# Optimization experiments

Hardware: AMD Instinct MI355X
Metric: run time of the kernel (lower is better)

Reference implementation:

```python
import jax, jax.numpy as jnp
import numpy as np

TOKENS = 8192
MODEL_DIM = 4096
PROMPT_DIM = 64
NUM_EXPERTS = 8
TOP_K = 2
EPS = float(np.finfo(np.float32).eps)


def setup_inputs() -> dict:
    key = jax.random.key(0)
    k1, k2, k3 = jax.random.split(key, 3)
    x = jax.random.normal(k1, (TOKENS, MODEL_DIM), dtype=jnp.float32)
    prompt = jax.random.normal(k2, (TOKENS, PROMPT_DIM), dtype=jnp.float32)
    # gate linear: Linear(model_dim + prompt_dim, num_experts, bias=True)
    W = jax.random.normal(k3, (MODEL_DIM + PROMPT_DIM, NUM_EXPERTS), dtype=jnp.float32) * 0.02
    b = jnp.zeros((NUM_EXPERTS,), dtype=jnp.float32)
    return {"x": x, "prompt": prompt, "W": W, "b": b}


def reference(x, prompt, W, b):
    # eval path: no jitter, no noise (self.training is False)
    logits = jnp.concatenate([x, prompt], axis=-1) @ W + b          # [T, E]
    _, topk_idx = jax.lax.top_k(logits, TOP_K)                      # [T, K]
    masks = jax.nn.one_hot(topk_idx, NUM_EXPERTS, dtype=jnp.float32)  # [T, K, E]
    gates = jax.nn.softmax(logits, axis=-1)                         # [T, E]
    gates_s = jnp.einsum("te,tke->tk", gates, masks)               # masked gather-sum
    if TOP_K > 1:
        denom = jnp.maximum(gates_s.sum(axis=-1, keepdims=True), EPS)
        gates_s = gates_s / denom
    # masks[:, i] == masks_se[i], gates_s[:, i] == gates_s[i] in the torch code
    return masks, gates_s
```

## Files before the change

kernel.cpp:

```cpp
#include <hip/hip_runtime.h>
#include <math.h>

#define NE 8
#define KDIM 4096
#define PDIM 64
#define WROWS (KDIM + PDIM)
#define EPS_F32 1.1920929e-07f
#define NCHUNK 16
#define TPW 2
#define WAVES 16
#define ROWF4 (WROWS / 4)
#define LDSF4 (NE * ROWF4)

typedef float f4 __attribute__((ext_vector_type(4)));

__global__ __launch_bounds__(256)
void transpose_w(const float* __restrict__ W, float* __restrict__ Wt) {
    const int k = blockIdx.x * 256 + threadIdx.x;
    if (k < WROWS) {
        float v[NE];
#pragma unroll
        for (int e = 0; e < NE; ++e) v[e] = W[(size_t)k * NE + e];
#pragma unroll
        for (int e = 0; e < NE; ++e) Wt[(size_t)e * WROWS + k] = v[e];
    }
}

__global__ __launch_bounds__(1024, 4)
void topk_gate(const float* __restrict__ x,
               const float* __restrict__ prompt,
               const float* __restrict__ Wt,
               const float* __restrict__ b,
               float* __restrict__ out,
               int tokens)
{
    __shared__ f4 wlds[LDSF4];

    const int tid  = threadIdx.x;
    const int lane = tid & 63;
    const int wid  = tid >> 6;

    {
        const f4* wt4 = (const f4*)Wt;
        for (int i = tid; i < LDSF4; i += WAVES * 64)
            wlds[i] = wt4[i];
    }
    __syncthreads();

    const int tbase = (blockIdx.x * WAVES + wid) * TPW;
    const int phase = (blockIdx.x * 5) & 15;

    float acc[TPW][NE];
#pragma unroll
    for (int t = 0; t < TPW; ++t)
#pragma unroll
        for (int e = 0; e < NE; ++e) acc[t][e] = 0.f;

    const f4* xr0 = (const f4*)(x + (size_t)tbase * KDIM);
    const f4* xr1 = (const f4*)(x + (size_t)(tbase + 1) * KDIM);

    f4 xb[3][TPW];

    auto cidx = [&](int c) { return ((c + phase) & 15) * 64 + lane; };

    {
        const int k0 = cidx(0);
        xb[0][0] = __builtin_nontemporal_load(xr0 + k0);
        xb[0][1] = __builtin_nontemporal_load(xr1 + k0);
        const int k1 = cidx(1);
        xb[1][0] = __builtin_nontemporal_load(xr0 + k1);
        xb[1][1] = __builtin_nontemporal_load(xr1 + k1);
    }

#pragma unroll
    for (int c = 0; c < NCHUNK; ++c) {
        if (c + 2 < NCHUNK) {
            const int kx = cidx(c + 2);
            xb[(c + 2) % 3][0] = __builtin_nontemporal_load(xr0 + kx);
            xb[(c + 2) % 3][1] = __builtin_nontemporal_load(xr1 + kx);
        }

        const int kw = cidx(c);
        f4 wb[NE];
#pragma unroll
        for (int e = 0; e < NE; ++e)
            wb[e] = wlds[e * ROWF4 + kw];

        const int s = c % 3;
#pragma unroll
        for (int t = 0; t < TPW; ++t)
#pragma unroll
            for (int e = 0; e < NE; ++e) {
                const f4 xv = xb[s][t];
                acc[t][e] = fmaf(xv.x, wb[e].x, acc[t][e]);
                acc[t][e] = fmaf(xv.y, wb[e].y, acc[t][e]);
                acc[t][e] = fmaf(xv.z, wb[e].z, acc[t][e]);
                acc[t][e] = fmaf(xv.w, wb[e].w, acc[t][e]);
            }
    }

    if (lane < 16) {
        f4 pv[TPW];
#pragma unroll
        for (int t = 0; t < TPW; ++t)
            pv[t] = *((const f4*)(prompt + (size_t)(tbase + t) * PDIM) + lane);
#pragma unroll
        for (int e = 0; e < NE; ++e) {
            const f4 wv = wlds[e * ROWF4 + (KDIM / 4) + lane];
#pragma unroll
            for (int t = 0; t < TPW; ++t) {
                acc[t][e] = fmaf(pv[t].x, wv.x, acc[t][e]);
                acc[t][e] = fmaf(pv[t].y, wv.y, acc[t][e]);
                acc[t][e] = fmaf(pv[t].z, wv.z, acc[t][e]);
                acc[t][e] = fmaf(pv[t].w, wv.w, acc[t][e]);
            }
        }
    }

#pragma unroll
    for (int t = 0; t < TPW; ++t)
#pragma unroll
        for (int e = 0; e < NE; ++e) {
            float v = acc[t][e];
#pragma unroll
            for (int off = 32; off >= 1; off >>= 1)
                v += __shfl_xor(v, off, 64);
            acc[t][e] = v;
        }

    const int tt = (lane >> 4) & 1;
    const int kk = (lane >> 3) & 1;
    const int ee = lane & 7;

    float lg[NE];
#pragma unroll
    for (int e = 0; e < NE; ++e) {
        const float v = (tt == 0) ? acc[0][e] : acc[1][e];
        lg[e] = v + b[e];
    }

    float v0 = lg[0]; int i0 = 0;
#pragma unroll
    for (int e = 1; e < NE; ++e)
        if (lg[e] > v0) { v0 = lg[e]; i0 = e; }
    float v1 = (i0 == 0) ? lg[1] : lg[0];
    int   i1 = (i0 == 0) ? 1 : 0;
#pragma unroll
    for (int e = 0; e < NE; ++e)
        if (e != i0 && lg[e] > v1) { v1 = lg[e]; i1 = e; }

    float s = 0.f;
#pragma unroll
    for (int e = 0; e < NE; ++e) s += __expf(lg[e] - v0);
    const float g0 = 1.0f / s;
    const float g1 = __expf(v1 - v0) / s;
    const float denom = fmaxf(g0 + g1, EPS_F32);

    if (lane < 32) {
        const int sel = kk ? i1 : i0;
        const int t_global = tbase + tt;
        out[(size_t)t_global * 16 + kk * 8 + ee] = (ee == sel) ? 1.0f : 0.0f;

        if ((lane & 15) < 2) {
            const float g = (ee == 0) ? (g0 / denom) : (g1 / denom);
            out[(size_t)tokens * 16 + (size_t)t_global * 2 + ee] = g;
        }
    }
}

extern "C" void kernel_launch(void* const* d_in, const int* in_sizes, int n_in,
                              void* d_out, int out_size, void* d_ws, size_t ws_size,
                              hipStream_t stream) {
    const float* x      = (const float*)d_in[0];
    const float* prompt = (const float*)d_in[1];
    const float* W      = (const float*)d_in[2];
    const float* b      = (const float*)d_in[3];
    float* out          = (float*)d_out;
    float* Wt           = (float*)d_ws;

    const int tokens = in_sizes[0] / KDIM;

    hipLaunchKernelGGL(transpose_w, dim3((WROWS + 255) / 256), dim3(256), 0, stream,
                       W, Wt);
    hipLaunchKernelGGL(topk_gate, dim3(tokens / (WAVES * TPW)), dim3(WAVES * 64),
                       0, stream, x, prompt, Wt, b, out, tokens);
}
```

Before: 202.4 us.

## Fuse weight transpose into gate kernel and prefetch x before LDS fill

Removes the separate transpose kernel launch. Each block now reads the original row-major W and scatters it transposed into shared memory. The first two x chunks are issued before the LDS fill, so global loads overlap the weight staging. The main loop now walks 8 groups of two 64-lane chunks instead of 16 chunks, with more x registers in flight. The trade-offs are scalar LDS stores, which may cause bank conflicts, higher register pressure, and every block redoing the transpose work.

```diff
diff --git a/kernel.cpp b/kernel.cpp
--- a/kernel.cpp
+++ b/kernel.cpp
@@ -6,97 +6,121 @@
 #define PDIM 64
 #define WROWS (KDIM + PDIM)
 #define EPS_F32 1.1920929e-07f
-#define NCHUNK 16
+#define NG 8
 #define TPW 2
 #define WAVES 16
 #define ROWF4 (WROWS / 4)
-#define LDSF4 (NE * ROWF4)
+#define LDSF (NE * WROWS)
 
 typedef float f4 __attribute__((ext_vector_type(4)));
-
-__global__ __launch_bounds__(256)
-void transpose_w(const float* __restrict__ W, float* __restrict__ Wt) {
-    const int k = blockIdx.x * 256 + threadIdx.x;
-    if (k < WROWS) {
-        float v[NE];
-#pragma unroll
-        for (int e = 0; e < NE; ++e) v[e] = W[(size_t)k * NE + e];
-#pragma unroll
-        for (int e = 0; e < NE; ++e) Wt[(size_t)e * WROWS + k] = v[e];
-    }
-}
 
 __global__ __launch_bounds__(1024, 4)
 void topk_gate(const float* __restrict__ x,
                const float* __restrict__ prompt,
-               const float* __restrict__ Wt,
+               const float* __restrict__ W,
                const float* __restrict__ b,
                float* __restrict__ out,
                int tokens)
 {
-    __shared__ f4 wlds[LDSF4];
+    __shared__ float wlds[LDSF];
 
     const int tid  = threadIdx.x;
     const int lane = tid & 63;
     const int wid  = tid >> 6;
 
-    {
-        const f4* wt4 = (const f4*)Wt;
-        for (int i = tid; i < LDSF4; i += WAVES * 64)
-            wlds[i] = wt4[i];
-    }
-    __syncthreads();
-
     const int tbase = (blockIdx.x * WAVES + wid) * TPW;
-    const int phase = (blockIdx.x * 5) & 15;
-
-    float acc[TPW][NE];
-#pragma unroll
-    for (int t = 0; t < TPW; ++t)
-#pragma unroll
-        for (int e = 0; e < NE; ++e) acc[t][e] = 0.f;
+    const int phase = (blockIdx.x * 5) & 7;
 
     const f4* xr0 = (const f4*)(x + (size_t)tbase * KDIM);
     const f4* xr1 = (const f4*)(x + (size_t)(tbase + 1) * KDIM);
 
-    f4 xb[3][TPW];
-
-    auto cidx = [&](int c) { return ((c + phase) & 15) * 64 + lane; };
+    f4 xb[3][TPW][2];
+
+    auto gidx = [&](int g, int j) {
+        return ((g + phase) & 7) * 128 + j * 64 + lane;
+    };
 
     {
-        const int k0 = cidx(0);
-        xb[0][0] = __builtin_nontemporal_load(xr0 + k0);
-        xb[0][1] = __builtin_nontemporal_load(xr1 + k0);
-        const int k1 = cidx(1);
-        xb[1][0] = __builtin_nontemporal_load(xr0 + k1);
-        xb[1][1] = __builtin_nontemporal_load(xr1 + k1);
-    }
-
-#pragma unroll
-    for (int c = 0; c < NCHUNK; ++c) {
-        if (c + 2 < NCHUNK) {
-            const int kx = cidx(c + 2);
-            xb[(c + 2) % 3][0] = __builtin_nontemporal_load(xr0 + kx);
-            xb[(c + 2) % 3][1] = __builtin_nontemporal_load(xr1 + kx);
-        }
-
-        const int kw = cidx(c);
-        f4 wb[NE];
-#pragma unroll
-        for (int e = 0; e < NE; ++e)
-            wb[e] = wlds[e * ROWF4 + kw];
-
-        const int s = c % 3;
-#pragma unroll
-        for (int t = 0; t < TPW; ++t)
-#pragma unroll
-            for (int e = 0; e < NE; ++e) {
-                const f4 xv = xb[s][t];
-                acc[t][e] = fmaf(xv.x, wb[e].x, acc[t][e]);
-                acc[t][e] = fmaf(xv.y, wb[e].y, acc[t][e]);
-                acc[t][e] = fmaf(xv.z, wb[e].z, acc[t][e]);
-                acc[t][e] = fmaf(xv.w, wb[e].w, acc[t][e]);
+        xb[0][0][0] = __builtin_nontemporal_load(xr0 + gidx(0, 0));
+        xb[0][0][1] = __builtin_nontemporal_load(xr0 + gidx(0, 1));
+        xb[0][1][0] = __builtin_nontemporal_load(xr1 + gidx(0, 0));
+        xb[0][1][1] = __builtin_nontemporal_load(xr1 + gidx(0, 1));
+        xb[1][0][0] = __builtin_nontemporal_load(xr0 + gidx(1, 0));
+        xb[1][0][1] = __builtin_nontemporal_load(xr0 + gidx(1, 1));
+        xb[1][1][0] = __builtin_nontemporal_load(xr1 + gidx(1, 0));
+        xb[1][1][1] = __builtin_nontemporal_load(xr1 + gidx(1, 1));
+    }
+
+    {
+        const f4* w4 = (const f4*)W;
+#pragma unroll
+        for (int it = 0; it < 4; ++it) {
+            const int k = tid + it * 1024;
+            const f4 a = w4[(size_t)k * 2];
+            const f4 c = w4[(size_t)k * 2 + 1];
+            wlds[0 * WROWS + k] = a.x;
+            wlds[1 * WROWS + k] = a.y;
+            wlds[2 * WROWS + k] = a.z;
+            wlds[3 * WROWS + k] = a.w;
+            wlds[4 * WROWS + k] = c.x;
+            wlds[5 * WROWS + k] = c.y;
+            wlds[6 * WROWS + k] = c.z;
+            wlds[7 * WROWS + k] = c.w;
+        }
+        if (tid < WROWS - 4096) {
+            const int k = tid + 4096;
+            const f4 a = w4[(size_t)k * 2];
+            const f4 c = w4[(size_t)k * 2 + 1];
+            wlds[0 * WROWS + k] = a.x;
+            wlds[1 * WROWS + k] = a.y;
+            wlds[2 * WROWS + k] = a.z;
+            wlds[3 * WROWS + k] = a.w;
+            wlds[4 * WROWS + k] = c.x;
+            wlds[5 * WROWS + k] = c.y;
+            wlds[6 * WROWS + k] = c.z;
+            wlds[7 * WROWS + k] = c.w;
+        }
+    }
+    __syncthreads();
+
+    float acc[TPW][NE];
+#pragma unroll
+    for (int t = 0; t < TPW; ++t)
+#pragma unroll
+        for (int e = 0; e < NE; ++e) acc[t][e] = 0.f;
+
+    const f4* wlds4 = (const f4*)wlds;
+
+#pragma unroll
+    for (int g = 0; g < NG; ++g) {
+        if (g + 2 < NG) {
+            const int bu = (g + 2) % 3;
+            xb[bu][0][0] = __builtin_nontemporal_load(xr0 + gidx(g + 2, 0));
+            xb[bu][0][1] = __builtin_nontemporal_load(xr0 + gidx(g + 2, 1));
+            xb[bu][1][0] = __builtin_nontemporal_load(xr1 + gidx(g + 2, 0));
+            xb[bu][1][1] = __builtin_nontemporal_load(xr1 + gidx(g + 2, 1));
+        }
+
+        const int s = g % 3;
+#pragma unroll
+        for (int j = 0; j < 2; ++j) {
+            const int kw = gidx(g, j);
+            f4 wb[NE];
+#pragma unroll
+            for (int e = 0; e < NE; ++e)
+                wb[e] = wlds4[e * ROWF4 + kw];
+#pragma unroll
+            for (int t = 0; t < TPW; ++t) {
+                const f4 xv = xb[s][t][j];
+#pragma unroll
+                for (int e = 0; e < NE; ++e) {
+                    acc[t][e] = fmaf(xv.x, wb[e].x, acc[t][e]);
+                    acc[t][e] = fmaf(xv.y, wb[e].y, acc[t][e]);
+                    acc[t][e] = fmaf(xv.z, wb[e].z, acc[t][e]);
+                    acc[t][e] = fmaf(xv.w, wb[e].w, acc[t][e]);
+                }
             }
+        }
     }
 
     if (lane < 16) {
@@ -106,7 +130,7 @@
             pv[t] = *((const f4*)(prompt + (size_t)(tbase + t) * PDIM) + lane);
 #pragma unroll
         for (int e = 0; e < NE; ++e) {
-            const f4 wv = wlds[e * ROWF4 + (KDIM / 4) + lane];
+            const f4 wv = wlds4[e * ROWF4 + (KDIM / 4) + lane];
 #pragma unroll
             for (int t = 0; t < TPW; ++t) {
                 acc[t][e] = fmaf(pv[t].x, wv.x, acc[t][e]);
@@ -176,12 +200,10 @@
     const float* W      = (const float*)d_in[2];
     const float* b      = (const float*)d_in[3];
     float* out          = (float*)d_out;
-    float* Wt           = (float*)d_ws;
+    (void)d_ws; (void)ws_size;
 
     const int tokens = in_sizes[0] / KDIM;
 
-    hipLaunchKernelGGL(transpose_w, dim3((WROWS + 255) / 256), dim3(256), 0, stream,
-                       W, Wt);
     hipLaunchKernelGGL(topk_gate, dim3(tokens / (WAVES * TPW)), dim3(WAVES * 64),
-                       0, stream, x, prompt, Wt, b, out, tokens);
+                       0, stream, x, prompt, W, b, out, tokens);
 }
```

Measured after the change: 214.8 us. 6.1% more time.

## Issue first x loads before W staging and use rolled rotating-register loop

Applied to the files above, without the earlier changes.

Moves the first two chunks of x global loads ahead of the LDS fill of the transposed weight matrix and __syncthreads, so HBM latency overlaps the weight staging. The main loop is made non-unrolled and uses rotating register buffers (a, b, n) instead of a 3-slot unrolled array. This cuts code size and register pressure at 1024-thread blocks, at the cost of loop overhead and less freedom for the compiler to schedule loads and FMAs across iterations.

```diff
diff --git a/kernel.cpp b/kernel.cpp
--- a/kernel.cpp
+++ b/kernel.cpp
@@ -40,6 +40,24 @@
     const int lane = tid & 63;
     const int wid  = tid >> 6;
 
+    const int tbase = (blockIdx.x * WAVES + wid) * TPW;
+    const int phase = (blockIdx.x * 5) & 15;
+
+    const f4* xr0 = (const f4*)(x + (size_t)tbase * KDIM);
+    const f4* xr1 = (const f4*)(x + (size_t)(tbase + 1) * KDIM);
+
+    auto cidx = [&](int c) { return ((c + phase) & 15) * 64 + lane; };
+
+    f4 a0, a1, b0, b1;
+    {
+        const int k0 = cidx(0);
+        a0 = __builtin_nontemporal_load(xr0 + k0);
+        a1 = __builtin_nontemporal_load(xr1 + k0);
+        const int k1 = cidx(1);
+        b0 = __builtin_nontemporal_load(xr0 + k1);
+        b1 = __builtin_nontemporal_load(xr1 + k1);
+    }
+
     {
         const f4* wt4 = (const f4*)Wt;
         for (int i = tid; i < LDSF4; i += WAVES * 64)
@@ -47,37 +65,19 @@
     }
     __syncthreads();
 
-    const int tbase = (blockIdx.x * WAVES + wid) * TPW;
-    const int phase = (blockIdx.x * 5) & 15;
-
     float acc[TPW][NE];
 #pragma unroll
     for (int t = 0; t < TPW; ++t)
 #pragma unroll
         for (int e = 0; e < NE; ++e) acc[t][e] = 0.f;
 
-    const f4* xr0 = (const f4*)(x + (size_t)tbase * KDIM);
-    const f4* xr1 = (const f4*)(x + (size_t)(tbase + 1) * KDIM);
-
-    f4 xb[3][TPW];
-
-    auto cidx = [&](int c) { return ((c + phase) & 15) * 64 + lane; };
-
-    {
-        const int k0 = cidx(0);
-        xb[0][0] = __builtin_nontemporal_load(xr0 + k0);
-        xb[0][1] = __builtin_nontemporal_load(xr1 + k0);
-        const int k1 = cidx(1);
-        xb[1][0] = __builtin_nontemporal_load(xr0 + k1);
-        xb[1][1] = __builtin_nontemporal_load(xr1 + k1);
-    }
-
-#pragma unroll
+#pragma unroll 1
     for (int c = 0; c < NCHUNK; ++c) {
+        f4 n0 = b0, n1 = b1;
         if (c + 2 < NCHUNK) {
             const int kx = cidx(c + 2);
-            xb[(c + 2) % 3][0] = __builtin_nontemporal_load(xr0 + kx);
-            xb[(c + 2) % 3][1] = __builtin_nontemporal_load(xr1 + kx);
+            n0 = __builtin_nontemporal_load(xr0 + kx);
+            n1 = __builtin_nontemporal_load(xr1 + kx);
         }
 
         const int kw = cidx(c);
@@ -86,17 +86,20 @@
         for (int e = 0; e < NE; ++e)
             wb[e] = wlds[e * ROWF4 + kw];
 
-        const int s = c % 3;
 #pragma unroll
-        for (int t = 0; t < TPW; ++t)
-#pragma unroll
-            for (int e = 0; e < NE; ++e) {
-                const f4 xv = xb[s][t];
-                acc[t][e] = fmaf(xv.x, wb[e].x, acc[t][e]);
-                acc[t][e] = fmaf(xv.y, wb[e].y, acc[t][e]);
-                acc[t][e] = fmaf(xv.z, wb[e].z, acc[t][e]);
-                acc[t][e] = fmaf(xv.w, wb[e].w, acc[t][e]);
-            }
+        for (int e = 0; e < NE; ++e) {
+            acc[0][e] = fmaf(a0.x, wb[e].x, acc[0][e]);
+            acc[0][e] = fmaf(a0.y, wb[e].y, acc[0][e]);
+            acc[0][e] = fmaf(a0.z, wb[e].z, acc[0][e]);
+            acc[0][e] = fmaf(a0.w, wb[e].w, acc[0][e]);
+            acc[1][e] = fmaf(a1.x, wb[e].x, acc[1][e]);
+            acc[1][e] = fmaf(a1.y, wb[e].y, acc[1][e]);
+            acc[1][e] = fmaf(a1.z, wb[e].z, acc[1][e]);
+            acc[1][e] = fmaf(a1.w, wb[e].w, acc[1][e]);
+        }
+
+        a0 = b0; a1 = b1;
+        b0 = n0; b1 = n1;
     }
 
     if (lane < 16) {
```

New measurement: 200.2 us. Within noise of the previous version (-1.1%).
